# Kernel tuning notes

Measured on AMD Instinct MI355X. Metric: run time of the kernel, lower is better.

Reference implementation:

```python
import jax, jax.numpy as jnp
import numpy as np

B, T, D_IN, D_OUT, H = 128, 128, 64, 64, 1024


def _lstm_cell(x_t, h, c, W_ih, W_hh, b_ih, b_hh):
    # PyTorch LSTMCell: gates = x@W_ih^T + b_ih + h@W_hh^T + b_hh, order [i, f, g, o]
    g = x_t @ W_ih.T + b_ih + h @ W_hh.T + b_hh  # [B, 4H]
    i, f, gg, o = jnp.split(g, 4, axis=-1)
    c_new = jax.nn.sigmoid(f) * c + jax.nn.sigmoid(i) * jnp.tanh(gg)
    h_new = jax.nn.sigmoid(o) * jnp.tanh(c_new)
    return h_new, c_new


def setup_inputs() -> dict:
    key = jax.random.key(0)
    ks = jax.random.split(key, 16)
    s_in = 1.0 / np.sqrt(H)
    inp = {
        "x": jax.random.normal(ks[0], (B, T, D_IN), dtype=jnp.float32),
        "W_ih1": jax.random.normal(ks[1], (4 * H, D_IN), dtype=jnp.float32) * s_in,
        "W_hh1": jax.random.normal(ks[2], (4 * H, H), dtype=jnp.float32) * s_in,
        "b_ih1": jax.random.normal(ks[3], (4 * H,), dtype=jnp.float32) * s_in,
        "b_hh1": jax.random.normal(ks[4], (4 * H,), dtype=jnp.float32) * s_in,
        "W_ih2": jax.random.normal(ks[5], (4 * H, H), dtype=jnp.float32) * s_in,
        "W_hh2": jax.random.normal(ks[6], (4 * H, H), dtype=jnp.float32) * s_in,
        "b_ih2": jax.random.normal(ks[7], (4 * H,), dtype=jnp.float32) * s_in,
        "b_hh2": jax.random.normal(ks[8], (4 * H,), dtype=jnp.float32) * s_in,
        "W_lin": jax.random.normal(ks[9], (D_IN, H), dtype=jnp.float32) * s_in,
        "b_lin": jax.random.normal(ks[10], (D_IN,), dtype=jnp.float32) * s_in,
        "W_hio": jax.random.normal(ks[11], (D_OUT, H), dtype=jnp.float32) * s_in,
        "b_hio": jax.random.normal(ks[12], (D_OUT,), dtype=jnp.float32) * s_in,
        "future": 1,
    }
    return inp


def reference(x, W_ih1, W_hh1, b_ih1, b_hh1, W_ih2, W_hh2, b_ih2, b_hh2,
              W_lin, b_lin, W_hio, b_hio, future):
    b = x.shape[0]
    h1 = jnp.zeros((b, H), x.dtype)
    c1 = jnp.zeros((b, H), x.dtype)
    h2 = jnp.zeros((b, H), x.dtype)
    c2 = jnp.zeros((b, H), x.dtype)

    def step(carry, x_t):
        h1, c1, h2, c2 = carry
        h1, c1 = _lstm_cell(x_t, h1, c1, W_ih1, W_hh1, b_ih1, b_hh1)
        h2, c2 = _lstm_cell(h1, h2, c2, W_ih2, W_hh2, b_ih2, b_hh2)
        return (h1, c1, h2, c2), None

    (h1, c1, h2, c2), _ = jax.lax.scan(step, (h1, c1, h2, c2),
                                       jnp.swapaxes(x, 0, 1))  # scan over T
    output = h2 @ W_lin.T + b_lin  # [B, D_IN] (only last step's value is used)

    for _ in range(int(future)):
        h1, c1 = _lstm_cell(output, h1, c1, W_ih1, W_hh1, b_ih1, b_hh1)
        h2, c2 = _lstm_cell(h1, h2, c2, W_ih2, W_hh2, b_ih2, b_hh2)
        output = h2 @ W_hio.T + b_hio  # [B, D_OUT]

    return output[:, None, :]  # [B, 1, D_OUT]
```

## Files before the change

kernel.cpp:

```cpp
#include <hip/hip_runtime.h>

#define B_   128
#define T_   128
#define DIN  64
#define H_   1024
#define NBLK 256
#define NTHR 512

typedef _Float16 f16;
typedef _Float16 half8 __attribute__((ext_vector_type(8)));
typedef float float4v __attribute__((ext_vector_type(4)));
typedef unsigned uint2v __attribute__((ext_vector_type(2)));
typedef unsigned uint4v __attribute__((ext_vector_type(4)));


#define OFF_W2   34816
#define OFF_SG1  100352
#define OFF_SG2  109056
#define OFF_C1   117760
#define OFF_C2   119808
#define OFF_B1   121856
#define OFF_B2   121920
#define SMEM_BYTES 121984


struct Params {
  const float *x, *Wih1, *Whh1, *bih1, *bhh1, *Wih2, *Whh2, *bih2, *bhh2,
              *Wlin, *blin, *Whio, *bhio;
  const int* fut;
  float* out;
  f16 *x16, *h1a, *h1b, *h2a, *h2b, *ob;
  unsigned *arrive, *rel;
  unsigned *S;
};

__device__ __forceinline__ float sigm(float v) { return 1.f / (1.f + __expf(-v)); }
__device__ __forceinline__ float tanh_(float v) { return 2.f / (1.f + __expf(-2.f * v)) - 1.f; }

__device__ __forceinline__ unsigned get_xcc() {
  unsigned x;
  asm volatile("s_getreg_b32 %0, hwreg(HW_REG_XCC_ID)" : "=s"(x));
  return x & 15u;
}

__device__ __forceinline__ void grid_sync(unsigned* arrive, unsigned* rel, unsigned ph) {
  __syncthreads();
  const int tid = threadIdx.x, bid = blockIdx.x;
  if (bid == 0) {
    if (tid > 0 && tid < NBLK) {
      while (__hip_atomic_load(&arrive[tid], __ATOMIC_RELAXED, __HIP_MEMORY_SCOPE_AGENT) != ph)
        __builtin_amdgcn_s_sleep(8);
    }
    __syncthreads();
    if (tid == 0)
      __hip_atomic_store(rel, ph, __ATOMIC_RELEASE, __HIP_MEMORY_SCOPE_AGENT);
  } else {
    if (tid == 0) {
      __hip_atomic_store(&arrive[bid], ph, __ATOMIC_RELEASE, __HIP_MEMORY_SCOPE_AGENT);
      while (__hip_atomic_load(rel, __ATOMIC_RELAXED, __HIP_MEMORY_SCOPE_AGENT) != ph)
        __builtin_amdgcn_s_sleep(8);
    }
  }
  __syncthreads();
  __builtin_amdgcn_fence(__ATOMIC_ACQUIRE, "agent");
}

__device__ __forceinline__ void fast_sync(unsigned* S, unsigned x, unsigned xtotal,
                                          unsigned nxcd, unsigned ph) {
  __syncthreads();
  if (threadIdx.x == 0) {
    unsigned t = __hip_atomic_fetch_add(&S[x * 32], 1u, __ATOMIC_RELAXED, __HIP_MEMORY_SCOPE_AGENT);
    bool leader = (t % xtotal == 0u);
    if ((t + 1u) % xtotal == 0u) {
      unsigned c = __hip_atomic_fetch_add(&S[512], 1u, __ATOMIC_RELAXED, __HIP_MEMORY_SCOPE_AGENT);
      if ((c + 1u) % nxcd == 0u)
        __hip_atomic_store(&S[544], ph, __ATOMIC_RELAXED, __HIP_MEMORY_SCOPE_AGENT);
      asm volatile("buffer_inv sc0 sc1\n\ts_waitcnt vmcnt(0)" ::: "memory");
      __hip_atomic_store(&S[1088 + x * 32], ph, __ATOMIC_RELAXED, __HIP_MEMORY_SCOPE_AGENT);
    }
    if (leader) {
      while (__hip_atomic_load(&S[544], __ATOMIC_RELAXED, __HIP_MEMORY_SCOPE_AGENT) != ph)
        __builtin_amdgcn_s_sleep(1);
      while (__hip_atomic_load(&S[1088 + x * 32], __ATOMIC_RELAXED, __HIP_MEMORY_SCOPE_AGENT) != ph)
        __builtin_amdgcn_s_sleep(1);
      __hip_atomic_store(&S[576 + x * 32], ph, __ATOMIC_RELAXED, __HIP_MEMORY_SCOPE_AGENT);
      asm volatile("buffer_inv sc0\n\ts_waitcnt vmcnt(0)" ::: "memory");
    } else {
      while (__hip_atomic_load(&S[576 + x * 32], __ATOMIC_RELAXED, __HIP_MEMORY_SCOPE_AGENT) != ph)
        __builtin_amdgcn_s_sleep(2);
      asm volatile("buffer_inv sc0\n\ts_waitcnt vmcnt(0)" ::: "memory");
    }
  }
  __syncthreads();
}

__global__ void __launch_bounds__(NTHR, 1) lstm_k(Params p) {
  extern __shared__ char smem[];
  f16*   W1s  = (f16*)(smem);
  f16*   W2s  = (f16*)(smem + OFF_W2);
  float* Sg1  = (float*)(smem + OFF_SG1);
  float* Sg2  = (float*)(smem + OFF_SG2);
  float* c1   = (float*)(smem + OFF_C1);
  float* c2   = (float*)(smem + OFF_C2);
  float* bs1  = (float*)(smem + OFF_B1);
  float* bs2  = (float*)(smem + OFF_B2);

  const int tid = threadIdx.x, bid = blockIdx.x;
  const int hb  = bid * 4;
  const int fut = p.fut[0];
  const unsigned xcc = get_xcc();
  unsigned* S = p.S;

  if (bid == 0) {
    for (int i = tid; i < 2048; i += NTHR)
      __hip_atomic_store(&S[i], 0u, __ATOMIC_RELAXED, __HIP_MEMORY_SCOPE_AGENT);
  }

  for (int idx = tid; idx < 34 * 512; idx += NTHR) {
    int c = idx >> 9, r = idx & 511;
    int q = r >> 7, colw = (r >> 3) & 15, j = r & 7;
    int k = c * 32 + q * 8 + j;
    int row = (colw >> 2) * H_ + hb + (colw & 3);
    float v = (k < H_) ? p.Whh1[row * H_ + k] : p.Wih1[row * DIN + (k - H_)];
    W1s[idx] = (f16)v;
  }
  for (int idx = tid; idx < 64 * 512; idx += NTHR) {
    int c = idx >> 9, r = idx & 511;
    int q = r >> 7, colw = (r >> 3) & 15, j = r & 7;
    int k = c * 32 + q * 8 + j;
    int row = (colw >> 2) * H_ + hb + (colw & 3);
    float v = (k < H_) ? p.Wih2[row * H_ + k] : p.Whh2[row * H_ + (k - H_)];
    W2s[idx] = (f16)v;
  }
  if (tid < 16) {
    int row = (tid >> 2) * H_ + hb + (tid & 3);
    bs1[tid] = p.bih1[row] + p.bhh1[row];
    bs2[tid] = p.bih2[row] + p.bhh2[row];
  }
  for (int i = tid; i < 512; i += NTHR) { c1[i] = 0.f; c2[i] = 0.f; }
  for (int i = bid * NTHR + tid; i < B_ * T_ * DIN; i += NBLK * NTHR)
    p.x16[i] = (f16)p.x[i];
  for (int i = bid * NTHR + tid; i < B_ * H_; i += NBLK * NTHR) {
    p.h1a[i] = (f16)0.f; p.h1b[i] = (f16)0.f;
    p.h2a[i] = (f16)0.f; p.h2b[i] = (f16)0.f;
  }

  unsigned ph = 1;
  grid_sync(p.arrive, p.rel, ph);
  if (tid == 0)
    __hip_atomic_fetch_add(&S[1600 + xcc], 1u, __ATOMIC_RELAXED, __HIP_MEMORY_SCOPE_AGENT);
  ++ph;
  grid_sync(p.arrive, p.rel, ph);

  unsigned xtotal = __hip_atomic_load(&S[1600 + xcc], __ATOMIC_RELAXED, __HIP_MEMORY_SCOPE_AGENT);
  unsigned nxcd = 0;
  for (int i = 0; i < 16; ++i)
    nxcd += (__hip_atomic_load(&S[1600 + i], __ATOMIC_RELAXED, __HIP_MEMORY_SCOPE_AGENT) != 0u);

  auto gsync = [&]() { ++ph; fast_sync(S, xcc, xtotal, nxcd, ph); };

  const int lane = tid & 63, wv = tid >> 6;
  const int col = lane & 15, quad = lane >> 4;
  const int m0 = wv * 16 + col;
  const int ko = quad * 8;
  const float b1v = bs1[col], b2v = bs2[col];
  const f16* W1f = W1s + lane * 8;
  const f16* W2f = W2s + lane * 8;
  const int hoff = quad * 1024 + m0 * 4;

  f16 *h1c = p.h1a, *h1n = p.h1b, *h2c = p.h2a, *h2n = p.h2b;

  auto lstm_pw = [&](const float* Sgb, float* cst, f16* hn) {
    int mm = tid >> 2, cc = tid & 3;
    float gi = Sgb[mm * 17 + cc],     gf = Sgb[mm * 17 + 4 + cc];
    float gg = Sgb[mm * 17 + 8 + cc], go = Sgb[mm * 17 + 12 + cc];
    float cn = sigm(gf) * cst[tid] + sigm(gi) * tanh_(gg);
    cst[tid] = cn;
    f16 hv = (f16)(sigm(go) * tanh_(cn));
    int v = (int)__builtin_bit_cast(unsigned short, hv);
    int base = lane & ~3;
    int v0 = __shfl(v, base, 64),     v1 = __shfl(v, base + 1, 64);
    int v2 = __shfl(v, base + 2, 64), v3 = __shfl(v, base + 3, 64);
    if (cc == 0) {
      unsigned long long pk = (unsigned long long)(unsigned short)v0
        | ((unsigned long long)(unsigned short)v1 << 16)
        | ((unsigned long long)(unsigned short)v2 << 32)
        | ((unsigned long long)(unsigned short)v3 << 48);
      __hip_atomic_store((unsigned long long*)(hn + bid * 512 + mm * 4), pk,
                         __ATOMIC_RELAXED, __HIP_MEMORY_SCOPE_AGENT);
    }
  };

  auto ldwin = [&](const f16* hX, int j) -> half8 {
    const uint2v* q0 = (const uint2v*)(hX + j * 4096 + hoff);
    const uint2v* q1 = (const uint2v*)(hX + j * 4096 + hoff + 512);
    uint2v u0 = *q0, u1 = *q1;
    uint4v u = {u0[0], u0[1], u1[0], u1[1]};
    return __builtin_bit_cast(half8, u);
  };

  auto phase = [&](bool l1, bool l2, const f16* xp, int xstr) {
    float4v a1 = {b1v, b1v, b1v, b1v};
    float4v a2 = {b2v, b2v, b2v, b2v};

    if (l1) {
      half8 ax0 = *(const half8*)(xp + m0 * xstr + ko);
      half8 ax1 = *(const half8*)(xp + m0 * xstr + 32 + ko);
      a1 = __builtin_amdgcn_mfma_f32_16x16x32_f16(ax0, *(const half8*)(W1f + 32 * 512), a1, 0, 0, 0);
      a1 = __builtin_amdgcn_mfma_f32_16x16x32_f16(ax1, *(const half8*)(W1f + 33 * 512), a1, 0, 0, 0);
    }
    if (l1 && l2) {
      #pragma unroll 4
      for (int j = 0; j < 32; ++j) {
        half8 aw = ldwin(h1c, j);
        a1 = __builtin_amdgcn_mfma_f32_16x16x32_f16(aw, *(const half8*)(W1f + j * 512), a1, 0, 0, 0);
        a2 = __builtin_amdgcn_mfma_f32_16x16x32_f16(aw, *(const half8*)(W2f + j * 512), a2, 0, 0, 0);
      }
    } else if (l1) {
      #pragma unroll 4
      for (int j = 0; j < 32; ++j) {
        half8 aw = ldwin(h1c, j);
        a1 = __builtin_amdgcn_mfma_f32_16x16x32_f16(aw, *(const half8*)(W1f + j * 512), a1, 0, 0, 0);
      }
    } else {
      #pragma unroll 4
      for (int j = 0; j < 32; ++j) {
        half8 aw = ldwin(h1c, j);
        a2 = __builtin_amdgcn_mfma_f32_16x16x32_f16(aw, *(const half8*)(W2f + j * 512), a2, 0, 0, 0);
      }
    }
    if (l2) {
      #pragma unroll 4
      for (int j = 0; j < 32; ++j) {
        half8 aw = ldwin(h2c, j);
        a2 = __builtin_amdgcn_mfma_f32_16x16x32_f16(aw, *(const half8*)(W2f + (32 + j) * 512), a2, 0, 0, 0);
      }
    }

    __syncthreads();
    if (l1) {
      #pragma unroll
      for (int r = 0; r < 4; ++r)
        Sg1[(wv * 16 + quad * 4 + r) * 17 + col] = a1[r];
    }
    if (l2) {
      #pragma unroll
      for (int r = 0; r < 4; ++r)
        Sg2[(wv * 16 + quad * 4 + r) * 17 + col] = a2[r];
    }
    __syncthreads();
    if (l1) lstm_pw(Sg1, c1, h1n);
    if (l2) lstm_pw(Sg2, c2, h2n);
  };

  auto out_phase = [&](const float* W, const float* bv, bool wout) {
    int j = bid & 63, mgp = bid >> 6;
    int rid = tid >> 4, ks = tid & 15;
    int mrow = mgp * 32 + rid;
    const float* wr = W + j * H_ + ks * 64;
    float s = 0.f;
    #pragma unroll
    for (int q = 0; q < 16; ++q) {
      const uint2v* hp = (const uint2v*)(h2c + (ks * 16 + q) * 512 + mrow * 4);
      uint2v u = *hp;
      half8 hv4;
      { uint4v t = {u[0], u[1], 0u, 0u}; hv4 = __builtin_bit_cast(half8, t); }
      s += (float)hv4[0] * wr[q * 4 + 0] + (float)hv4[1] * wr[q * 4 + 1]
         + (float)hv4[2] * wr[q * 4 + 2] + (float)hv4[3] * wr[q * 4 + 3];
    }
    s += __shfl_down(s, 8, 16);
    s += __shfl_down(s, 4, 16);
    s += __shfl_down(s, 2, 16);
    s += __shfl_down(s, 1, 16);
    if (ks == 0) {
      float v = s + bv[j];
      f16 hv = (f16)v;
      __hip_atomic_store((unsigned short*)&p.ob[mrow * 64 + j],
                         __builtin_bit_cast(unsigned short, hv),
                         __ATOMIC_RELAXED, __HIP_MEMORY_SCOPE_AGENT);
      if (wout) p.out[mrow * 64 + j] = v;
    }
  };

  for (int t = -1; t < T_; ++t) {
    bool l1 = (t + 1 < T_), l2 = (t >= 0);
    phase(l1, l2, p.x16 + (t + 1) * DIN, T_ * DIN);
    gsync();
    if (l1) { f16* tm = h1c; h1c = h1n; h1n = tm; }
    if (l2) { f16* tm = h2c; h2c = h2n; h2n = tm; }
  }
  out_phase(p.Wlin, p.blin, fut == 0);
  gsync();
  for (int f = 0; f < fut; ++f) {
    phase(true, false, p.ob, 64);
    gsync();
    { f16* tm = h1c; h1c = h1n; h1n = tm; }
    phase(false, true, p.ob, 64);
    gsync();
    { f16* tm = h2c; h2c = h2n; h2n = tm; }
    out_phase(p.Whio, p.bhio, f == fut - 1);
    gsync();
  }
}

extern "C" void kernel_launch(void* const* d_in, const int* in_sizes, int n_in,
                              void* d_out, int out_size, void* d_ws, size_t ws_size,
                              hipStream_t stream) {
  char* w = (char*)d_ws;
  auto carve = [&](size_t n) { char* r = w; w += (n + 255) & ~(size_t)255; return r; };

  Params p;
  p.x    = (const float*)d_in[0];
  p.Wih1 = (const float*)d_in[1];
  p.Whh1 = (const float*)d_in[2];
  p.bih1 = (const float*)d_in[3];
  p.bhh1 = (const float*)d_in[4];
  p.Wih2 = (const float*)d_in[5];
  p.Whh2 = (const float*)d_in[6];
  p.bih2 = (const float*)d_in[7];
  p.bhh2 = (const float*)d_in[8];
  p.Wlin = (const float*)d_in[9];
  p.blin = (const float*)d_in[10];
  p.Whio = (const float*)d_in[11];
  p.bhio = (const float*)d_in[12];
  p.fut  = (const int*)d_in[13];
  p.out  = (float*)d_out;

  p.x16 = (f16*)carve((size_t)B_ * T_ * DIN * 2);
  p.h1a = (f16*)carve((size_t)B_ * H_ * 2);
  p.h1b = (f16*)carve((size_t)B_ * H_ * 2);
  p.h2a = (f16*)carve((size_t)B_ * H_ * 2);
  p.h2b = (f16*)carve((size_t)B_ * H_ * 2);
  p.ob  = (f16*)carve((size_t)B_ * 64 * 2);
  p.arrive = (unsigned*)carve(NBLK * sizeof(unsigned));
  p.rel    = (unsigned*)carve(256);
  p.S      = (unsigned*)carve(2048 * sizeof(unsigned));

  (void)hipFuncSetAttribute((const void*)lstm_k,
                            hipFuncAttributeMaxDynamicSharedMemorySize, SMEM_BYTES);
  void* args[] = { &p };
  (void)hipLaunchCooperativeKernel((void*)lstm_k, dim3(NBLK), dim3(NTHR),
                                   args, SMEM_BYTES, stream);
}
```

Baseline: 1.918 ms.

## Split recurrent K-reduction across two wave groups with 1024 threads per block

```diff
diff --git a/kernel.cpp b/kernel.cpp
--- a/kernel.cpp
+++ b/kernel.cpp
@@ -5,7 +5,7 @@
 #define DIN  64
 #define H_   1024
 #define NBLK 256
-#define NTHR 512
+#define NTHR 1024
 
 typedef _Float16 f16;
 typedef _Float16 half8 __attribute__((ext_vector_type(8)));
@@ -14,14 +14,16 @@
 typedef unsigned uint4v __attribute__((ext_vector_type(4)));
 
 
-#define OFF_W2   34816
-#define OFF_SG1  100352
-#define OFF_SG2  109056
-#define OFF_C1   117760
-#define OFF_C2   119808
-#define OFF_B1   121856
-#define OFF_B2   121920
-#define SMEM_BYTES 121984
+#define OFF_W2    34816
+#define OFF_SG1A  100352
+#define OFF_SG1B  109056
+#define OFF_SG2A  117760
+#define OFF_SG2B  126464
+#define OFF_C1    135168
+#define OFF_C2    137216
+#define OFF_B1    139264
+#define OFF_B2    139328
+#define SMEM_BYTES 139392
 
 
 struct Params {
@@ -94,12 +96,14 @@
   __syncthreads();
 }
 
-__global__ void __launch_bounds__(NTHR, 1) lstm_k(Params p) {
+__global__ void __launch_bounds__(NTHR, 4) lstm_k(Params p) {
   extern __shared__ char smem[];
   f16*   W1s  = (f16*)(smem);
   f16*   W2s  = (f16*)(smem + OFF_W2);
-  float* Sg1  = (float*)(smem + OFF_SG1);
-  float* Sg2  = (float*)(smem + OFF_SG2);
+  float* Sg1A = (float*)(smem + OFF_SG1A);
+  float* Sg1B = (float*)(smem + OFF_SG1B);
+  float* Sg2A = (float*)(smem + OFF_SG2A);
+  float* Sg2B = (float*)(smem + OFF_SG2B);
   float* c1   = (float*)(smem + OFF_C1);
   float* c2   = (float*)(smem + OFF_C2);
   float* bs1  = (float*)(smem + OFF_B1);
@@ -159,21 +163,30 @@
 
   auto gsync = [&]() { ++ph; fast_sync(S, xcc, xtotal, nxcd, ph); };
 
-  const int lane = tid & 63, wv = tid >> 6;
+  const int lane = tid & 63, wq = tid >> 6;
+  const int g  = wq >> 3;
+  const int wv = wq & 7;
   const int col = lane & 15, quad = lane >> 4;
   const int m0 = wv * 16 + col;
   const int ko = quad * 8;
-  const float b1v = bs1[col], b2v = bs2[col];
+  const int jb = g * 16;
+  const float b1v = g ? 0.f : bs1[col];
+  const float b2v = g ? 0.f : bs2[col];
   const f16* W1f = W1s + lane * 8;
   const f16* W2f = W2s + lane * 8;
+  float* S1w = g ? Sg1B : Sg1A;
+  float* S2w = g ? Sg2B : Sg2A;
   const int hoff = quad * 1024 + m0 * 4;
 
   f16 *h1c = p.h1a, *h1n = p.h1b, *h2c = p.h2a, *h2n = p.h2b;
 
-  auto lstm_pw = [&](const float* Sgb, float* cst, f16* hn) {
+  auto lstm_pw = [&](const float* SgA, const float* SgB, float* cst, f16* hn) {
     int mm = tid >> 2, cc = tid & 3;
-    float gi = Sgb[mm * 17 + cc],     gf = Sgb[mm * 17 + 4 + cc];
-    float gg = Sgb[mm * 17 + 8 + cc], go = Sgb[mm * 17 + 12 + cc];
+    int i0 = mm * 17 + cc;
+    float gi = SgA[i0]      + SgB[i0];
+    float gf = SgA[i0 + 4]  + SgB[i0 + 4];
+    float gg = SgA[i0 + 8]  + SgB[i0 + 8];
+    float go = SgA[i0 + 12] + SgB[i0 + 12];
     float cn = sigm(gf) * cst[tid] + sigm(gi) * tanh_(gg);
     cst[tid] = cn;
     f16 hv = (f16)(sigm(go) * tanh_(cn));
@@ -204,36 +217,34 @@
     float4v a2 = {b2v, b2v, b2v, b2v};
 
     if (l1) {
-      half8 ax0 = *(const half8*)(xp + m0 * xstr + ko);
-      half8 ax1 = *(const half8*)(xp + m0 * xstr + 32 + ko);
-      a1 = __builtin_amdgcn_mfma_f32_16x16x32_f16(ax0, *(const half8*)(W1f + 32 * 512), a1, 0, 0, 0);
-      a1 = __builtin_amdgcn_mfma_f32_16x16x32_f16(ax1, *(const half8*)(W1f + 33 * 512), a1, 0, 0, 0);
+      half8 ax = *(const half8*)(xp + m0 * xstr + g * 32 + ko);
+      a1 = __builtin_amdgcn_mfma_f32_16x16x32_f16(ax, *(const half8*)(W1f + (32 + g) * 512), a1, 0, 0, 0);
     }
     if (l1 && l2) {
-      #pragma unroll 4
-      for (int j = 0; j < 32; ++j) {
-        half8 aw = ldwin(h1c, j);
-        a1 = __builtin_amdgcn_mfma_f32_16x16x32_f16(aw, *(const half8*)(W1f + j * 512), a1, 0, 0, 0);
-        a2 = __builtin_amdgcn_mfma_f32_16x16x32_f16(aw, *(const half8*)(W2f + j * 512), a2, 0, 0, 0);
+      #pragma unroll
+      for (int i = 0; i < 16; ++i) {
+        int j = jb + i;
+        half8 w1 = ldwin(h1c, j);
+        half8 w2 = ldwin(h2c, j);
+        a1 = __builtin_amdgcn_mfma_f32_16x16x32_f16(w1, *(const half8*)(W1f + j * 512), a1, 0, 0, 0);
+        a2 = __builtin_amdgcn_mfma_f32_16x16x32_f16(w1, *(const half8*)(W2f + j * 512), a2, 0, 0, 0);
+        a2 = __builtin_amdgcn_mfma_f32_16x16x32_f16(w2, *(const half8*)(W2f + (32 + j) * 512), a2, 0, 0, 0);
       }
     } else if (l1) {
-      #pragma unroll 4
-      for (int j = 0; j < 32; ++j) {
-        half8 aw = ldwin(h1c, j);
-        a1 = __builtin_amdgcn_mfma_f32_16x16x32_f16(aw, *(const half8*)(W1f + j * 512), a1, 0, 0, 0);
+      #pragma unroll
+      for (int i = 0; i < 16; ++i) {
+        int j = jb + i;
+        half8 w1 = ldwin(h1c, j);
+        a1 = __builtin_amdgcn_mfma_f32_16x16x32_f16(w1, *(const half8*)(W1f + j * 512), a1, 0, 0, 0);
       }
-    } else {
-      #pragma unroll 4
-      for (int j = 0; j < 32; ++j) {
-        half8 aw = ldwin(h1c, j);
-        a2 = __builtin_amdgcn_mfma_f32_16x16x32_f16(aw, *(const half8*)(W2f + j * 512), a2, 0, 0, 0);
-      }
-    }
-    if (l2) {
-      #pragma unroll 4
-      for (int j = 0; j < 32; ++j) {
-        half8 aw = ldwin(h2c, j);
-        a2 = __builtin_amdgcn_mfma_f32_16x16x32_f16(aw, *(const half8*)(W2f + (32 + j) * 512), a2, 0, 0, 0);
+    } else if (l2) {
+      #pragma unroll
+      for (int i = 0; i < 16; ++i) {
+        int j = jb + i;
+        half8 w1 = ldwin(h1c, j);
+        half8 w2 = ldwin(h2c, j);
+        a2 = __builtin_amdgcn_mfma_f32_16x16x32_f16(w1, *(const half8*)(W2f + j * 512), a2, 0, 0, 0);
+        a2 = __builtin_amdgcn_mfma_f32_16x16x32_f16(w2, *(const half8*)(W2f + (32 + j) * 512), a2, 0, 0, 0);
       }
     }
 
@@ -241,19 +252,22 @@
     if (l1) {
       #pragma unroll
       for (int r = 0; r < 4; ++r)
-        Sg1[(wv * 16 + quad * 4 + r) * 17 + col] = a1[r];
+        S1w[(wv * 16 + quad * 4 + r) * 17 + col] = a1[r];
     }
     if (l2) {
       #pragma unroll
       for (int r = 0; r < 4; ++r)
-        Sg2[(wv * 16 + quad * 4 + r) * 17 + col] = a2[r];
+        S2w[(wv * 16 + quad * 4 + r) * 17 + col] = a2[r];
     }
     __syncthreads();
-    if (l1) lstm_pw(Sg1, c1, h1n);
-    if (l2) lstm_pw(Sg2, c2, h2n);
+    if (tid < 512) {
+      if (l1) lstm_pw(Sg1A, Sg1B, c1, h1n);
+      if (l2) lstm_pw(Sg2A, Sg2B, c2, h2n);
+    }
   };
 
   auto out_phase = [&](const float* W, const float* bv, bool wout) {
+    if (tid >= 512) return;
     int j = bid & 63, mgp = bid >> 6;
     int rid = tid >> 4, ks = tid & 15;
     int mrow = mgp * 32 + rid;
```

Result: no change. 1.897 ms (-1.1%).
